# Kernel optimization log

Measured on AMD Instinct MI355X. Metric: run time of the kernel, lower is better.

Reference implementation:

```python
import jax, jax.numpy as jnp
import numpy as np

HID = 768
INTER = 3072
H = 12
DH = 64
N = 16384
W = 256   # attention_width
L = 512   # per-sequence length (power of 2, used via the uint32 bit-mask trick)


def rotate_every_two(x):
    x1 = x[..., ::2]
    x2 = x[..., 1::2]
    return jnp.stack((-x2, x1), axis=-1).reshape(x.shape)


def setup_inputs() -> dict:
    key = jax.random.key(0)
    ks = jax.random.split(key, 6)
    # GPT-J style interleaved rotary tables: sin/cos each value repeated twice
    inv_freq = 1.0 / (10000.0 ** (np.arange(0, DH, 2) / DH))  # [DH/2]
    ang = np.arange(N)[:, None] * inv_freq[None, :]           # [N, DH/2]
    pos_sin = jnp.asarray(np.repeat(np.sin(ang), 2, axis=-1), dtype=jnp.float32)
    pos_cos = jnp.asarray(np.repeat(np.cos(ang), 2, axis=-1), dtype=jnp.float32)
    return {
        "x": jax.random.normal(ks[0], (N, HID), dtype=jnp.float32),
        "normed_ages": jax.random.normal(ks[1], (N,), dtype=jnp.float32),
        "pos_sin": pos_sin,
        "pos_cos": pos_cos,
        "ln_scale": jnp.ones((HID,), dtype=jnp.float32),
        "ln_offset": jnp.zeros((HID,), dtype=jnp.float32),
        "w_in": jax.random.normal(ks[2], (HID, 3 * HID + INTER), dtype=jnp.float32) * 0.02,
        "b_in": jnp.zeros((3 * HID + INTER,), dtype=jnp.float32),
        "w_out": jax.random.normal(ks[3], (HID + INTER, HID), dtype=jnp.float32) * 0.02,
        "b_out": jnp.zeros((HID,), dtype=jnp.float32),
        "length": L,
    }


def reference(x, normed_ages, pos_sin, pos_cos, ln_scale, ln_offset,
              w_in, b_in, w_out, b_out, length):
    # LayerNorm (haiku: eps=1e-5, create_scale/offset)
    mu = jnp.mean(x, axis=-1, keepdims=True)
    var = jnp.var(x, axis=-1, keepdims=True)
    xn = (x - mu) * jax.lax.rsqrt(var + 1e-5) * ln_scale + ln_offset

    # fused QKV + FF projection (note: original computes x_with_ages but never uses it)
    mid = xn @ w_in + b_in
    q, k, v, ff = jnp.split(mid, [HID, 2 * HID, 3 * HID], axis=-1)

    def to_heads(t):  # [N, HID] -> [H, N, DH]
        return t.reshape(N, H, DH).transpose(1, 0, 2)

    q, k, v = to_heads(q), to_heads(k), to_heads(v)

    # rotary ('per_head'): sincos broadcast over heads
    sin, cos = pos_sin[None], pos_cos[None]
    q = q * cos + rotate_every_two(q) * sin
    k = k * cos + rotate_every_two(k) * sin

    # local (sliding-window, causal, within-sequence) attention, chunked by W
    C = W
    nc = N // C
    qc = q.reshape(H, nc, C, DH)
    kc = k.reshape(H, nc, C, DH)
    vc = v.reshape(H, nc, C, DH)
    kprev = jnp.concatenate([jnp.zeros_like(kc[:, :1]), kc[:, :-1]], axis=1)
    vprev = jnp.concatenate([jnp.zeros_like(vc[:, :1]), vc[:, :-1]], axis=1)
    kcat = jnp.concatenate([kprev, kc], axis=2)  # [H, nc, 2C, DH]
    vcat = jnp.concatenate([vprev, vc], axis=2)

    qi = (jnp.arange(nc) * C)[:, None] + jnp.arange(C)        # [nc, C]
    kj = (jnp.arange(nc) * C)[:, None] - C + jnp.arange(2 * C)  # [nc, 2C]
    lm = ~(jnp.uint32(length) - jnp.uint32(1))  # same bit-trick as the module
    same_seq = ((qi[:, :, None].astype(jnp.uint32) & lm) ==
                (jnp.maximum(kj, 0)[:, None, :].astype(jnp.uint32) & lm))
    d = qi[:, :, None] - kj[:, None, :]
    mask = (kj[:, None, :] >= 0) & (d >= 0) & (d < W) & same_seq  # [nc, C, 2C]

    scale = 1.0 / jnp.sqrt(jnp.float32(DH))
    scores = jnp.einsum('hncd,hnkd->hnck', qc, kcat) * scale
    scores = jnp.where(mask[None], scores, jnp.float32(-1e30))
    probs = jax.nn.softmax(scores, axis=-1)
    attn = jnp.einsum('hnck,hnkd->hncd', probs, vcat)

    attn = attn.reshape(H, N, DH).transpose(1, 0, 2).reshape(N, HID)
    combined = jnp.concatenate([attn, jax.nn.gelu(ff)], axis=-1)
    return xn + combined @ w_out + b_out
```

## Files before the change

### kernel.cpp

```cpp
#include <hip/hip_runtime.h>

#define N_TOK 16384
#define HIDN  768
#define MIDN  5376
#define COMBN 3840
#define NH    12
#define DHD   64
#define CHUNK 256
#define WIN   256

typedef short s16x8 __attribute__((ext_vector_type(8)));
typedef short s16x4 __attribute__((ext_vector_type(4)));
typedef float f32x4 __attribute__((ext_vector_type(4)));

__device__ __forceinline__ float bf2f(unsigned short u){
  union { unsigned u; float f; } x; x.u = ((unsigned)u) << 16; return x.f;
}
__device__ __forceinline__ unsigned short f2bf(float f){
  union { float f; unsigned u; } x; x.f = f;
  unsigned r = x.u + 0x7fffu + ((x.u >> 16) & 1u);
  return (unsigned short)(r >> 16);
}
__device__ __forceinline__ float gelu_fast(float x){
  float u = -1.5957691216057308f * (x + 0.044715f * x * x * x);
  return x / (1.f + __expf(u));
}
__device__ __forceinline__ void glds16(const void* g, void* l){
  __builtin_amdgcn_global_load_lds(
      (const __attribute__((address_space(1))) unsigned*)g,
      (__attribute__((address_space(3))) unsigned*)l, 16, 0, 0);
}

__global__ __launch_bounds__(256) void transpose_f2b(
    const float* __restrict__ in, unsigned short* __restrict__ out,
    int R, int Cc)
{
  __shared__ short t[64 * 72];
  const int tid = threadIdx.x;
  const int r0 = blockIdx.y * 64, c0 = blockIdx.x * 64;
  #pragma unroll
  for (int rep = 0; rep < 4; rep++){
    int v = tid + 256 * rep;
    int r = v >> 4, s = v & 15;
    float4 d = *(const float4*)(in + (size_t)(r0 + r) * Cc + c0 + s * 4);
    s16x4 o = { (short)f2bf(d.x), (short)f2bf(d.y), (short)f2bf(d.z), (short)f2bf(d.w) };
    *(s16x4*)(t + r * 72 + s * 4) = o;
  }
  __syncthreads();
  #pragma unroll
  for (int rep = 0; rep < 2; rep++){
    int v = tid + 256 * rep;
    int c = v & 63, s2 = v >> 6;
    s16x8 d;
    #pragma unroll
    for (int j = 0; j < 8; j++) d[j] = t[(s2 * 8 + j) * 72 + c];
    *(s16x8*)(out + (size_t)(c0 + c) * R + r0 + s2 * 8) = d;
  }
}

__global__ __launch_bounds__(256) void ln_kernel(
    const float* __restrict__ x, const float* __restrict__ sc,
    const float* __restrict__ ofs, unsigned short* __restrict__ xn)
{
  const int lane = threadIdx.x & 63, wv = threadIdx.x >> 6;
  const int row = blockIdx.x * 4 + wv;
  const float4* xr = (const float4*)(x + (size_t)row * HIDN);
  float4 vals[3];
  float sum = 0.f, sq = 0.f;
  #pragma unroll
  for (int j = 0; j < 3; j++){
    vals[j] = xr[lane + 64 * j];
    sum += vals[j].x + vals[j].y + vals[j].z + vals[j].w;
    sq  += vals[j].x * vals[j].x + vals[j].y * vals[j].y
         + vals[j].z * vals[j].z + vals[j].w * vals[j].w;
  }
  #pragma unroll
  for (int o = 1; o < 64; o <<= 1){ sum += __shfl_xor(sum, o); sq += __shfl_xor(sq, o); }
  const float mu = sum * (1.f / HIDN);
  const float rs = rsqrtf(fmaxf(sq * (1.f / HIDN) - mu * mu, 0.f) + 1e-5f);
  s16x4* xo = (s16x4*)(xn + (size_t)row * HIDN);
  const float4* scp = (const float4*)sc;
  const float4* ofp = (const float4*)ofs;
  #pragma unroll
  for (int j = 0; j < 3; j++){
    int p = lane + 64 * j;
    float4 s = scp[p], o = ofp[p];
    s16x4 w;
    w[0] = (short)f2bf((vals[j].x - mu) * rs * s.x + o.x);
    w[1] = (short)f2bf((vals[j].y - mu) * rs * s.y + o.y);
    w[2] = (short)f2bf((vals[j].z - mu) * rs * s.z + o.z);
    w[3] = (short)f2bf((vals[j].w - mu) * rs * s.w + o.w);
    xo[p] = w;
  }
}

__device__ __forceinline__ int swz(int row, int quad){
  return row * 64 + ((quad ^ ((row >> 1) & 3)) << 4);
}

__global__ __launch_bounds__(256, 2) void gemm1_k(
    const unsigned short* __restrict__ A, const unsigned short* __restrict__ BT,
    const float* __restrict__ bias,
    unsigned short* __restrict__ qb, unsigned short* __restrict__ kb,
    unsigned short* __restrict__ vb, unsigned short* __restrict__ comb)
{
  constexpr int K = HIDN;
  __shared__ short As[256 * 32];
  __shared__ short Bs[128 * 32];
  const int tid = threadIdx.x, lane = tid & 63, wv = tid >> 6;
  const int quad = lane >> 4, l15 = lane & 15;
  const int n0 = blockIdx.x * 128, m0 = blockIdx.y * 256;

  f32x4 acc[4][8];
  #pragma unroll
  for (int i = 0; i < 4; i++)
    #pragma unroll
    for (int j = 0; j < 8; j++) acc[i][j] = (f32x4){0.f,0.f,0.f,0.f};

  const int srow = tid >> 2;
  const int sseg = (tid & 3) ^ ((tid >> 3) & 3);
  const unsigned short* Ap = A  + (size_t)(m0 + srow) * K + sseg * 8;
  const unsigned short* Bp = BT + (size_t)(n0 + srow) * K + sseg * 8;
  const size_t rstep = (size_t)64 * K;
  char* AsB = ((char*)As) + tid * 16;
  char* BsB = ((char*)Bs) + tid * 16;

  int offA[4], offB[8];
  #pragma unroll
  for (int rt = 0; rt < 4; rt++) offA[rt] = swz(wv * 64 + rt * 16 + l15, quad);
  #pragma unroll
  for (int ct = 0; ct < 8; ct++) offB[ct] = swz(ct * 16 + l15, quad);

  for (int kt = 0; kt < K; kt += 32){
    __syncthreads();
    glds16(Ap + kt,             AsB);
    glds16(Ap + kt + rstep,     AsB + 4096);
    glds16(Ap + kt + 2 * rstep, AsB + 8192);
    glds16(Ap + kt + 3 * rstep, AsB + 12288);
    glds16(Bp + kt,             BsB);
    glds16(Bp + kt + rstep,     BsB + 4096);
    __syncthreads();
    s16x8 a[4], b[8];
    #pragma unroll
    for (int rt = 0; rt < 4; rt++) a[rt] = *(const s16x8*)((const char*)As + offA[rt]);
    #pragma unroll
    for (int ct = 0; ct < 8; ct++) b[ct] = *(const s16x8*)((const char*)Bs + offB[ct]);
    #pragma unroll
    for (int rt = 0; rt < 4; rt++)
      #pragma unroll
      for (int ct = 0; ct < 8; ct++)
        acc[rt][ct] = __builtin_amdgcn_mfma_f32_16x16x32_bf16(a[rt], b[ct], acc[rt][ct], 0, 0, 0);
  }

  unsigned short* dstb; int cb; bool isff = false;
  if (n0 < 768)       { dstb = qb;   cb = n0; }
  else if (n0 < 1536) { dstb = kb;   cb = n0 - 768; }
  else if (n0 < 2304) { dstb = vb;   cb = n0 - 1536; }
  else                { dstb = comb; cb = n0 - 1536; isff = true; }
  const int rowstride = isff ? COMBN : HIDN;

  #pragma unroll
  for (int ct = 0; ct < 8; ct++){
    const float bsv = bias[n0 + ct * 16 + l15];
    const int col = cb + ct * 16 + l15;
    #pragma unroll
    for (int rt = 0; rt < 4; rt++){
      #pragma unroll
      for (int r = 0; r < 4; r++){
        const int row = m0 + wv * 64 + rt * 16 + quad * 4 + r;
        float val = acc[rt][ct][r] + bsv;
        if (isff) val = gelu_fast(val);
        dstb[(size_t)row * rowstride + col] = f2bf(val);
      }
    }
  }
}

__global__ __launch_bounds__(256) void gemm2_k(
    const unsigned short* __restrict__ A, const unsigned short* __restrict__ BT,
    const float* __restrict__ bias, const unsigned short* __restrict__ xn,
    float* __restrict__ outp)
{
  constexpr int K = COMBN;
  __shared__ short As[128 * 32];
  __shared__ short Bs[128 * 32];
  const int tid = threadIdx.x, lane = tid & 63, wv = tid >> 6;
  const int quad = lane >> 4, l15 = lane & 15;
  const int m0 = blockIdx.y * 128, n0 = blockIdx.x * 128;
  const int wr = (wv >> 1) * 64, wc = (wv & 1) * 64;

  f32x4 acc[4][4];
  #pragma unroll
  for (int i = 0; i < 4; i++)
    #pragma unroll
    for (int j = 0; j < 4; j++) acc[i][j] = (f32x4){0.f,0.f,0.f,0.f};

  const int srow = tid >> 2;
  const int sseg = (tid & 3) ^ ((tid >> 3) & 3);
  const unsigned short* Ap = A  + (size_t)(m0 + srow) * K + sseg * 8;
  const unsigned short* Bp = BT + (size_t)(n0 + srow) * K + sseg * 8;
  const size_t rstep = (size_t)64 * K;
  char* AsB = ((char*)As) + tid * 16;
  char* BsB = ((char*)Bs) + tid * 16;

  int offA[4], offB[4];
  #pragma unroll
  for (int rt = 0; rt < 4; rt++) offA[rt] = swz(wr + rt * 16 + l15, quad);
  #pragma unroll
  for (int ct = 0; ct < 4; ct++) offB[ct] = swz(wc + ct * 16 + l15, quad);

  for (int kt = 0; kt < K; kt += 32){
    __syncthreads();
    glds16(Ap + kt,         AsB);
    glds16(Ap + kt + rstep, AsB + 4096);
    glds16(Bp + kt,         BsB);
    glds16(Bp + kt + rstep, BsB + 4096);
    __syncthreads();
    s16x8 a[4], b[4];
    #pragma unroll
    for (int rt = 0; rt < 4; rt++) a[rt] = *(const s16x8*)((const char*)As + offA[rt]);
    #pragma unroll
    for (int ct = 0; ct < 4; ct++) b[ct] = *(const s16x8*)((const char*)Bs + offB[ct]);
    #pragma unroll
    for (int rt = 0; rt < 4; rt++)
      #pragma unroll
      for (int ct = 0; ct < 4; ct++)
        acc[rt][ct] = __builtin_amdgcn_mfma_f32_16x16x32_bf16(a[rt], b[ct], acc[rt][ct], 0, 0, 0);
  }

  #pragma unroll
  for (int ct = 0; ct < 4; ct++){
    const int col = n0 + wc + ct * 16 + l15;
    const float bsv = bias[col];
    #pragma unroll
    for (int rt = 0; rt < 4; rt++){
      #pragma unroll
      for (int r = 0; r < 4; r++){
        const int row = m0 + wr + rt * 16 + quad * 4 + r;
        const size_t o = (size_t)row * HIDN + col;
        outp[o] = bf2f(xn[o]) + acc[rt][ct][r] + bsv;
      }
    }
  }
}

__global__ __launch_bounds__(384) void rope_qk(
    unsigned short* __restrict__ qb, unsigned short* __restrict__ kb,
    const float* __restrict__ psin, const float* __restrict__ pcos)
{
  __shared__ float ss[2048], cs[2048];
  const int tid = threadIdx.x, g = blockIdx.x;
  #pragma unroll
  for (int rep = 0; rep < 6; rep++){
    int idx = rep * 384 + tid;
    if (idx < 2048){
      int tok = idx >> 5, p = idx & 31;
      size_t gt = ((size_t)(g * 64 + tok)) * DHD + 2 * p;
      ss[idx] = psin[gt];
      cs[idx] = pcos[gt];
    }
  }
  __syncthreads();
  const int p = tid & 31;
  unsigned* q32 = (unsigned*)qb;
  unsigned* k32 = (unsigned*)kb;
  for (int tok = 0; tok < 64; tok++){
    const size_t a = ((size_t)(g * 64 + tok)) * 384 + tid;
    const float s = ss[tok * 32 + p], c0 = cs[tok * 32 + p];
    unsigned u = q32[a];
    float e = bf2f((unsigned short)(u & 0xffff));
    float d = bf2f((unsigned short)(u >> 16));
    q32[a] = (unsigned)f2bf((e * c0 - d * s) * 0.125f)
           | (((unsigned)f2bf((d * c0 + e * s) * 0.125f)) << 16);
    u = k32[a];
    e = bf2f((unsigned short)(u & 0xffff));
    d = bf2f((unsigned short)(u >> 16));
    k32[a] = (unsigned)f2bf(e * c0 - d * s)
           | (((unsigned)f2bf(d * c0 + e * s)) << 16);
  }
}

__global__ __launch_bounds__(256) void attn_kernel(
    const unsigned short* __restrict__ qb, const unsigned short* __restrict__ kb,
    const unsigned short* __restrict__ vb, unsigned short* __restrict__ comb,
    const int* __restrict__ lenp)
{
  __shared__ short Ks[2][64 * 72];
  __shared__ short Vt[2][64 * 64];
  __shared__ short Ps[4][16 * 72];
  const int tid = threadIdx.x, lane = tid & 63, wv = tid >> 6;
  const int quad = lane >> 4, l15 = lane & 15;
  const int h = blockIdx.y, c = blockIdx.x;
  const unsigned lm = ~((unsigned)lenp[0] - 1u);
  const int i0 = c * CHUNK + wv * 64;
  const unsigned short* qh = qb + h * DHD;
  const unsigned short* kh = kb + h * DHD;
  const unsigned short* vh = vb + h * DHD;

  s16x8 qf[4][2];
  #pragma unroll
  for (int rt = 0; rt < 4; rt++){
    const unsigned short* qr = qh + (size_t)(i0 + rt * 16 + l15) * HIDN;
    qf[rt][0] = *(const s16x8*)(qr + quad * 8);
    qf[rt][1] = *(const s16x8*)(qr + 32 + quad * 8);
  }

  f32x4 O[4][4];
  float mm[4][4], ll[4][4];
  #pragma unroll
  for (int rt = 0; rt < 4; rt++)
    #pragma unroll
    for (int j = 0; j < 4; j++){ O[rt][j] = (f32x4){0,0,0,0}; mm[rt][j] = -1e30f; ll[rt][j] = 0.f; }
  short* myP = &Ps[wv][0];

  const int skey = tid & 63, sseg = tid >> 6;
  const int jb0 = c * CHUNK - 256;
  s16x8 kr[2], vr[2];

  auto issue = [&](int jb){
    if (jb >= 0){
      const unsigned short* kp = kh + (size_t)(jb + skey) * HIDN + sseg * 16;
      const unsigned short* vp = vh + (size_t)(jb + skey) * HIDN + sseg * 16;
      kr[0] = *(const s16x8*)(kp);     kr[1] = *(const s16x8*)(kp + 8);
      vr[0] = *(const s16x8*)(vp);     vr[1] = *(const s16x8*)(vp + 8);
    } else {
      kr[0] = kr[1] = vr[0] = vr[1] = (s16x8){0,0,0,0,0,0,0,0};
    }
  };

  issue(jb0);
  for (int tb = 0; tb < 8; tb++){
    const int jb = jb0 + tb * 64;
    const int buf = tb & 1;
    short* Kb = &Ks[buf][0];
    short* Vb = &Vt[buf][0];
    *(s16x8*)(Kb + skey * 72 + sseg * 16)     = kr[0];
    *(s16x8*)(Kb + skey * 72 + sseg * 16 + 8) = kr[1];
    #pragma unroll
    for (int half = 0; half < 2; half++)
      #pragma unroll
      for (int j = 0; j < 8; j++){
        const int d = sseg * 16 + half * 8 + j;
        Vb[d * 64 + (((skey & 56) ^ ((d & 7) << 3)) | (skey & 7))] = vr[half][j];
      }
    if (tb < 7) issue(jb + 64);
    __syncthreads();

    const bool act = (jb >= 0) && (jb <= i0 + 63) && (jb + 63 >= i0 - 255) &&
                     (((unsigned)i0 & lm) == ((unsigned)jb & lm));
    if (!act) continue;

    #pragma unroll
    for (int rt = 0; rt < 4; rt++){
      const int ilo = i0 + rt * 16;
      if (ilo + 15 < jb || ilo - (jb + 63) >= WIN) continue;
      f32x4 sc[4];
      #pragma unroll
      for (int ct = 0; ct < 4; ct++){
        const short* kbase = Kb + (ct * 16 + l15) * 72 + quad * 8;
        const s16x8 b0 = *(const s16x8*)(kbase);
        const s16x8 b1 = *(const s16x8*)(kbase + 32);
        f32x4 a = (f32x4){0,0,0,0};
        a = __builtin_amdgcn_mfma_f32_16x16x32_bf16(qf[rt][0], b0, a, 0, 0, 0);
        a = __builtin_amdgcn_mfma_f32_16x16x32_bf16(qf[rt][1], b1, a, 0, 0, 0);
        sc[ct] = a;
      }
      float alph[4];
      #pragma unroll
      for (int r = 0; r < 4; r++){
        const int i = ilo + quad * 4 + r;
        #pragma unroll
        for (int ct = 0; ct < 4; ct++){
          const unsigned dd = (unsigned)(i - (jb + ct * 16 + l15));
          if (dd >= 256u) sc[ct][r] = -1e30f;
        }
        float mx = fmaxf(fmaxf(sc[0][r], sc[1][r]), fmaxf(sc[2][r], sc[3][r]));
        mx = fmaxf(mx, __shfl_xor(mx, 1));
        mx = fmaxf(mx, __shfl_xor(mx, 2));
        mx = fmaxf(mx, __shfl_xor(mx, 4));
        mx = fmaxf(mx, __shfl_xor(mx, 8));
        const float mnew = fmaxf(mm[rt][r], mx);
        alph[r] = __expf(mm[rt][r] - mnew);
        mm[rt][r] = mnew;
        float p0 = __expf(sc[0][r] - mnew);
        float p1 = __expf(sc[1][r] - mnew);
        float p2 = __expf(sc[2][r] - mnew);
        float p3 = __expf(sc[3][r] - mnew);
        sc[0][r] = p0; sc[1][r] = p1; sc[2][r] = p2; sc[3][r] = p3;
        float rsum = (p0 + p1) + (p2 + p3);
        rsum += __shfl_xor(rsum, 1);
        rsum += __shfl_xor(rsum, 2);
        rsum += __shfl_xor(rsum, 4);
        rsum += __shfl_xor(rsum, 8);
        ll[rt][r] = ll[rt][r] * alph[r] + rsum;
      }
      #pragma unroll
      for (int co = 0; co < 4; co++)
        #pragma unroll
        for (int r = 0; r < 4; r++) O[rt][co][r] *= alph[r];
      #pragma unroll
      for (int r = 0; r < 4; r++){
        const int prow = quad * 4 + r;
        #pragma unroll
        for (int ct = 0; ct < 4; ct++)
          myP[prow * 72 + ct * 16 + l15] = (short)f2bf(sc[ct][r]);
      }
      #pragma unroll
      for (int ks2 = 0; ks2 < 2; ks2++){
        const s16x8 pf = *(const s16x8*)(myP + l15 * 72 + ks2 * 32 + quad * 8);
        #pragma unroll
        for (int co = 0; co < 4; co++){
          const int d = co * 16 + l15;
          const s16x8 vf = *(const s16x8*)(Vb + d * 64 +
                              ((ks2 * 32 + quad * 8) ^ ((d & 7) << 3)));
          O[rt][co] = __builtin_amdgcn_mfma_f32_16x16x32_bf16(pf, vf, O[rt][co], 0, 0, 0);
        }
      }
    }
  }

  #pragma unroll
  for (int rt = 0; rt < 4; rt++)
    #pragma unroll
    for (int co = 0; co < 4; co++)
      #pragma unroll
      for (int r = 0; r < 4; r++){
        const int tok = i0 + rt * 16 + quad * 4 + r;
        comb[(size_t)tok * COMBN + h * DHD + co * 16 + l15] = f2bf(O[rt][co][r] / ll[rt][r]);
      }
}

extern "C" void kernel_launch(void* const* d_in, const int* in_sizes, int n_in,
                              void* d_out, int out_size, void* d_ws, size_t ws_size,
                              hipStream_t stream)
{
  const float* x     = (const float*)d_in[0];
  const float* psin  = (const float*)d_in[2];
  const float* pcos  = (const float*)d_in[3];
  const float* lns   = (const float*)d_in[4];
  const float* lno   = (const float*)d_in[5];
  const float* w_in  = (const float*)d_in[6];
  const float* b_in  = (const float*)d_in[7];
  const float* w_out = (const float*)d_in[8];
  const float* b_out = (const float*)d_in[9];
  const int*   lenp  = (const int*)d_in[10];
  float* out = (float*)d_out;

  char* ws = (char*)d_ws;
  size_t off = 0;
  unsigned short* xn    = (unsigned short*)(ws + off); off += (size_t)N_TOK * HIDN * 2;
  unsigned short* wInT  = (unsigned short*)(ws + off); off += (size_t)MIDN * HIDN * 2;
  unsigned short* wOutT = (unsigned short*)(ws + off); off += (size_t)HIDN * COMBN * 2;
  unsigned short* qbuf  = (unsigned short*)(ws + off); off += (size_t)N_TOK * HIDN * 2;
  unsigned short* kbuf  = (unsigned short*)(ws + off); off += (size_t)N_TOK * HIDN * 2;
  unsigned short* vbuf  = (unsigned short*)(ws + off); off += (size_t)N_TOK * HIDN * 2;
  unsigned short* comb  = (unsigned short*)(ws + off); off += (size_t)N_TOK * COMBN * 2;

  transpose_f2b<<<dim3(MIDN/64, HIDN/64), 256, 0, stream>>>(w_in, wInT, HIDN, MIDN);
  transpose_f2b<<<dim3(HIDN/64, COMBN/64), 256, 0, stream>>>(w_out, wOutT, COMBN, HIDN);
  ln_kernel<<<dim3(N_TOK/4), 256, 0, stream>>>(x, lns, lno, xn);
  gemm1_k<<<dim3(MIDN/128, N_TOK/256), 256, 0, stream>>>(
      xn, wInT, b_in, qbuf, kbuf, vbuf, comb);
  rope_qk<<<dim3(N_TOK/64), 384, 0, stream>>>(qbuf, kbuf, psin, pcos);
  attn_kernel<<<dim3(N_TOK/CHUNK, NH), 256, 0, stream>>>(
      qbuf, kbuf, vbuf, comb, lenp);
  gemm2_k<<<dim3(HIDN/128, N_TOK/128), 256, 0, stream>>>(
      comb, wOutT, b_out, xn, out);
}
```

Baseline: 699.1 us.

## Double-buffer LDS tiles in both GEMMs to overlap global loads with MFMA

Both GEMM kernels now hold two shared-memory tile buffers and issue the next K-tile's global-to-LDS loads before computing on the current tile. Explicit s_waitcnt vmcnt and s_barrier replace the two __syncthreads per iteration, so memory latency can overlap with MFMA work. This doubles LDS use per block, which may lower occupancy, especially in gemm1, which launches with two blocks per CU and already uses 24KB.

Measured after the change: 662.9 us. -5.2%, faster.

```diff
diff --git a/kernel.cpp b/kernel.cpp
--- a/kernel.cpp
+++ b/kernel.cpp
@@ -105,8 +105,9 @@
     unsigned short* __restrict__ vb, unsigned short* __restrict__ comb)
 {
   constexpr int K = HIDN;
-  __shared__ short As[256 * 32];
-  __shared__ short Bs[128 * 32];
+  constexpr int NKT = K / 32;
+  __shared__ short As[2][256 * 32];
+  __shared__ short Bs[2][128 * 32];
   const int tid = threadIdx.x, lane = tid & 63, wv = tid >> 6;
   const int quad = lane >> 4, l15 = lane & 15;
   const int n0 = blockIdx.x * 128, m0 = blockIdx.y * 256;
@@ -122,8 +123,8 @@
   const unsigned short* Ap = A  + (size_t)(m0 + srow) * K + sseg * 8;
   const unsigned short* Bp = BT + (size_t)(n0 + srow) * K + sseg * 8;
   const size_t rstep = (size_t)64 * K;
-  char* AsB = ((char*)As) + tid * 16;
-  char* BsB = ((char*)Bs) + tid * 16;
+  char* AsB[2] = { ((char*)As[0]) + tid * 16, ((char*)As[1]) + tid * 16 };
+  char* BsB[2] = { ((char*)Bs[0]) + tid * 16, ((char*)Bs[1]) + tid * 16 };
 
   int offA[4], offB[8];
   #pragma unroll
@@ -131,25 +132,46 @@
   #pragma unroll
   for (int ct = 0; ct < 8; ct++) offB[ct] = swz(ct * 16 + l15, quad);
 
-  for (int kt = 0; kt < K; kt += 32){
-    __syncthreads();
-    glds16(Ap + kt,             AsB);
-    glds16(Ap + kt + rstep,     AsB + 4096);
-    glds16(Ap + kt + 2 * rstep, AsB + 8192);
-    glds16(Ap + kt + 3 * rstep, AsB + 12288);
-    glds16(Bp + kt,             BsB);
-    glds16(Bp + kt + rstep,     BsB + 4096);
-    __syncthreads();
+  glds16(Ap,             AsB[0]);
+  glds16(Ap + rstep,     AsB[0] + 4096);
+  glds16(Ap + 2 * rstep, AsB[0] + 8192);
+  glds16(Ap + 3 * rstep, AsB[0] + 12288);
+  glds16(Bp,             BsB[0]);
+  glds16(Bp + rstep,     BsB[0] + 4096);
+
+  for (int t = 0; t < NKT; ++t){
+    const int buf = t & 1;
+    if (t + 1 < NKT){
+      const int kn = (t + 1) * 32;
+      char* Ad = AsB[buf ^ 1];
+      char* Bd = BsB[buf ^ 1];
+      glds16(Ap + kn,             Ad);
+      glds16(Ap + kn + rstep,     Ad + 4096);
+      glds16(Ap + kn + 2 * rstep, Ad + 8192);
+      glds16(Ap + kn + 3 * rstep, Ad + 12288);
+      glds16(Bp + kn,             Bd);
+      glds16(Bp + kn + rstep,     Bd + 4096);
+      asm volatile("s_waitcnt vmcnt(6)" ::: "memory");
+    } else {
+      asm volatile("s_waitcnt vmcnt(0)" ::: "memory");
+    }
+    asm volatile("s_barrier" ::: "memory");
+
+    const char* Ab = (const char*)As[buf];
+    const char* Bb = (const char*)Bs[buf];
     s16x8 a[4], b[8];
     #pragma unroll
-    for (int rt = 0; rt < 4; rt++) a[rt] = *(const s16x8*)((const char*)As + offA[rt]);
-    #pragma unroll
-    for (int ct = 0; ct < 8; ct++) b[ct] = *(const s16x8*)((const char*)Bs + offB[ct]);
+    for (int rt = 0; rt < 4; rt++) a[rt] = *(const s16x8*)(Ab + offA[rt]);
+    #pragma unroll
+    for (int ct = 0; ct < 8; ct++) b[ct] = *(const s16x8*)(Bb + offB[ct]);
     #pragma unroll
     for (int rt = 0; rt < 4; rt++)
       #pragma unroll
       for (int ct = 0; ct < 8; ct++)
         acc[rt][ct] = __builtin_amdgcn_mfma_f32_16x16x32_bf16(a[rt], b[ct], acc[rt][ct], 0, 0, 0);
+
+    asm volatile("s_waitcnt lgkmcnt(0)" ::: "memory");
+    asm volatile("s_barrier" ::: "memory");
   }
 
   unsigned short* dstb; int cb; bool isff = false;
@@ -182,8 +204,9 @@
     float* __restrict__ outp)
 {
   constexpr int K = COMBN;
-  __shared__ short As[128 * 32];
-  __shared__ short Bs[128 * 32];
+  constexpr int NKT = K / 32;
+  __shared__ short As[2][128 * 32];
+  __shared__ short Bs[2][128 * 32];
   const int tid = threadIdx.x, lane = tid & 63, wv = tid >> 6;
   const int quad = lane >> 4, l15 = lane & 15;
   const int m0 = blockIdx.y * 128, n0 = blockIdx.x * 128;
@@ -200,8 +223,8 @@
   const unsigned short* Ap = A  + (size_t)(m0 + srow) * K + sseg * 8;
   const unsigned short* Bp = BT + (size_t)(n0 + srow) * K + sseg * 8;
   const size_t rstep = (size_t)64 * K;
-  char* AsB = ((char*)As) + tid * 16;
-  char* BsB = ((char*)Bs) + tid * 16;
+  char* AsB[2] = { ((char*)As[0]) + tid * 16, ((char*)As[1]) + tid * 16 };
+  char* BsB[2] = { ((char*)Bs[0]) + tid * 16, ((char*)Bs[1]) + tid * 16 };
 
   int offA[4], offB[4];
   #pragma unroll
@@ -209,23 +232,42 @@
   #pragma unroll
   for (int ct = 0; ct < 4; ct++) offB[ct] = swz(wc + ct * 16 + l15, quad);
 
-  for (int kt = 0; kt < K; kt += 32){
-    __syncthreads();
-    glds16(Ap + kt,         AsB);
-    glds16(Ap + kt + rstep, AsB + 4096);
-    glds16(Bp + kt,         BsB);
-    glds16(Bp + kt + rstep, BsB + 4096);
-    __syncthreads();
+  glds16(Ap,         AsB[0]);
+  glds16(Ap + rstep, AsB[0] + 4096);
+  glds16(Bp,         BsB[0]);
+  glds16(Bp + rstep, BsB[0] + 4096);
+
+  for (int t = 0; t < NKT; ++t){
+    const int buf = t & 1;
+    if (t + 1 < NKT){
+      const int kn = (t + 1) * 32;
+      char* Ad = AsB[buf ^ 1];
+      char* Bd = BsB[buf ^ 1];
+      glds16(Ap + kn,         Ad);
+      glds16(Ap + kn + rstep, Ad + 4096);
+      glds16(Bp + kn,         Bd);
+      glds16(Bp + kn + rstep, Bd + 4096);
+      asm volatile("s_waitcnt vmcnt(4)" ::: "memory");
+    } else {
+      asm volatile("s_waitcnt vmcnt(0)" ::: "memory");
+    }
+    asm volatile("s_barrier" ::: "memory");
+
+    const char* Ab = (const char*)As[buf];
+    const char* Bb = (const char*)Bs[buf];
     s16x8 a[4], b[4];
     #pragma unroll
-    for (int rt = 0; rt < 4; rt++) a[rt] = *(const s16x8*)((const char*)As + offA[rt]);
-    #pragma unroll
-    for (int ct = 0; ct < 4; ct++) b[ct] = *(const s16x8*)((const char*)Bs + offB[ct]);
+    for (int rt = 0; rt < 4; rt++) a[rt] = *(const s16x8*)(Ab + offA[rt]);
+    #pragma unroll
+    for (int ct = 0; ct < 4; ct++) b[ct] = *(const s16x8*)(Bb + offB[ct]);
     #pragma unroll
     for (int rt = 0; rt < 4; rt++)
       #pragma unroll
       for (int ct = 0; ct < 4; ct++)
         acc[rt][ct] = __builtin_amdgcn_mfma_f32_16x16x32_bf16(a[rt], b[ct], acc[rt][ct], 0, 0, 0);
+
+    asm volatile("s_waitcnt lgkmcnt(0)" ::: "memory");
+    asm volatile("s_barrier" ::: "memory");
   }
 
   #pragma unroll
```

## Restructure both GEMMs into 256x256 double-buffered 8-wave tiles with prioritized MFMA phases

Applied to the files above, without the earlier changes.

Both projection GEMMs move to 256x256 output tiles with 512 threads (8 waves, 2x4 arrangement) and a 64-wide K step. Shared memory is double-buffered, and the next tile is prefetched with direct global-to-LDS loads overlapped with compute through vmcnt waits. The inner loop is split into four sub-phases with register reuse and s_setprio around the MFMA bursts. The aim is to hide global load latency and raise the compute-to-memory ratio. In exchange it uses 128KB of LDS per block, more accumulator registers, and launches fewer blocks: gemm1 gets 21 column blocks (MIDN/256), gemm2 only 3x64 blocks.

New measurement: 713.9 us. 2.1% more time.

```diff
diff --git a/kernel.cpp b/kernel.cpp
--- a/kernel.cpp
+++ b/kernel.cpp
@@ -94,62 +94,143 @@
   }
 }
 
-__device__ __forceinline__ int swz(int row, int quad){
-  return row * 64 + ((quad ^ ((row >> 1) & 3)) << 4);
-}
-
-__global__ __launch_bounds__(256, 2) void gemm1_k(
+
+__global__ __launch_bounds__(512, 2) void gemm1_k(
     const unsigned short* __restrict__ A, const unsigned short* __restrict__ BT,
     const float* __restrict__ bias,
     unsigned short* __restrict__ qb, unsigned short* __restrict__ kb,
     unsigned short* __restrict__ vb, unsigned short* __restrict__ comb)
 {
   constexpr int K = HIDN;
-  __shared__ short As[256 * 32];
-  __shared__ short Bs[128 * 32];
+  constexpr int T = K / 64;
+  __shared__ short As[2 * 256 * 64];
+  __shared__ short Bs[2 * 256 * 64];
   const int tid = threadIdx.x, lane = tid & 63, wv = tid >> 6;
   const int quad = lane >> 4, l15 = lane & 15;
-  const int n0 = blockIdx.x * 128, m0 = blockIdx.y * 256;
-
-  f32x4 acc[4][8];
-  #pragma unroll
-  for (int i = 0; i < 4; i++)
-    #pragma unroll
-    for (int j = 0; j < 8; j++) acc[i][j] = (f32x4){0.f,0.f,0.f,0.f};
-
-  const int srow = tid >> 2;
-  const int sseg = (tid & 3) ^ ((tid >> 3) & 3);
-  const unsigned short* Ap = A  + (size_t)(m0 + srow) * K + sseg * 8;
-  const unsigned short* Bp = BT + (size_t)(n0 + srow) * K + sseg * 8;
-  const size_t rstep = (size_t)64 * K;
-  char* AsB = ((char*)As) + tid * 16;
-  char* BsB = ((char*)Bs) + tid * 16;
-
-  int offA[4], offB[8];
-  #pragma unroll
-  for (int rt = 0; rt < 4; rt++) offA[rt] = swz(wv * 64 + rt * 16 + l15, quad);
-  #pragma unroll
-  for (int ct = 0; ct < 8; ct++) offB[ct] = swz(ct * 16 + l15, quad);
-
-  for (int kt = 0; kt < K; kt += 32){
-    __syncthreads();
-    glds16(Ap + kt,             AsB);
-    glds16(Ap + kt + rstep,     AsB + 4096);
-    glds16(Ap + kt + 2 * rstep, AsB + 8192);
-    glds16(Ap + kt + 3 * rstep, AsB + 12288);
-    glds16(Bp + kt,             BsB);
-    glds16(Bp + kt + rstep,     BsB + 4096);
-    __syncthreads();
-    s16x8 a[4], b[8];
-    #pragma unroll
-    for (int rt = 0; rt < 4; rt++) a[rt] = *(const s16x8*)((const char*)As + offA[rt]);
-    #pragma unroll
-    for (int ct = 0; ct < 8; ct++) b[ct] = *(const s16x8*)((const char*)Bs + offB[ct]);
-    #pragma unroll
-    for (int rt = 0; rt < 4; rt++)
-      #pragma unroll
-      for (int ct = 0; ct < 8; ct++)
-        acc[rt][ct] = __builtin_amdgcn_mfma_f32_16x16x32_bf16(a[rt], b[ct], acc[rt][ct], 0, 0, 0);
+  const int wr = wv >> 2, wc = wv & 3;
+  const int n0 = blockIdx.x * 256, m0 = blockIdx.y * 256;
+
+  f32x4 acc[8][4];
+  #pragma unroll
+  for (int i = 0; i < 8; i++)
+    #pragma unroll
+    for (int j = 0; j < 4; j++) acc[i][j] = (f32x4){0.f,0.f,0.f,0.f};
+
+  const int srow = tid >> 3;
+  const int koff = ((tid & 7) ^ ((tid >> 3) & 7)) * 8;
+  const unsigned short* Ap = A  + (size_t)(m0 + srow) * K + koff;
+  const unsigned short* Bp = BT + (size_t)(n0 + srow) * K + koff;
+  const size_t pstep = (size_t)64 * K;
+  char* const AsR = (char*)As;
+  char* const BsR = (char*)Bs;
+
+  const int seg0 = ((quad ^ (l15 & 7)) << 4);
+  const int seg1 = (((quad + 4) ^ (l15 & 7)) << 4);
+
+  auto stage = [&](int tt){
+    const int par = tt & 1;
+    char* Ad = AsR + par * 32768 + tid * 16;
+    char* Bd = BsR + par * 32768 + tid * 16;
+    const unsigned short* Asrc = Ap + tt * 64;
+    const unsigned short* Bsrc = Bp + tt * 64;
+    #pragma unroll
+    for (int part = 0; part < 4; part++)
+      glds16(Asrc + part * pstep, Ad + part * 8192);
+    #pragma unroll
+    for (int part = 0; part < 4; part++)
+      glds16(Bsrc + part * pstep, Bd + part * 8192);
+  };
+
+  stage(0);
+
+  s16x8 a[4][2], b[2][2];
+
+  #pragma unroll 2
+  for (int t = 0; t < T; t++){
+    const int par = t & 1;
+    const char* Ab = AsR + par * 32768;
+    const char* Bb = BsR + par * 32768;
+    if (t + 1 < T){
+      stage(t + 1);
+      asm volatile("s_waitcnt vmcnt(8)" ::: "memory");
+    } else {
+      asm volatile("s_waitcnt vmcnt(0)" ::: "memory");
+    }
+    asm volatile("s_barrier" ::: "memory");
+
+    #pragma unroll
+    for (int i = 0; i < 4; i++){
+      const char* rb = Ab + ((wr * 128 + i * 16 + l15) << 7);
+      a[i][0] = *(const s16x8*)(rb + seg0);
+      a[i][1] = *(const s16x8*)(rb + seg1);
+    }
+    #pragma unroll
+    for (int j = 0; j < 2; j++){
+      const char* rb = Bb + ((wc * 64 + j * 16 + l15) << 7);
+      b[j][0] = *(const s16x8*)(rb + seg0);
+      b[j][1] = *(const s16x8*)(rb + seg1);
+    }
+    __builtin_amdgcn_s_setprio(1);
+    #pragma unroll
+    for (int i = 0; i < 4; i++)
+      #pragma unroll
+      for (int j = 0; j < 2; j++){
+        acc[i][j] = __builtin_amdgcn_mfma_f32_16x16x32_bf16(a[i][0], b[j][0], acc[i][j], 0, 0, 0);
+        acc[i][j] = __builtin_amdgcn_mfma_f32_16x16x32_bf16(a[i][1], b[j][1], acc[i][j], 0, 0, 0);
+      }
+    __builtin_amdgcn_s_setprio(0);
+    asm volatile("s_barrier" ::: "memory");
+
+    #pragma unroll
+    for (int j = 0; j < 2; j++){
+      const char* rb = Bb + ((wc * 64 + (2 + j) * 16 + l15) << 7);
+      b[j][0] = *(const s16x8*)(rb + seg0);
+      b[j][1] = *(const s16x8*)(rb + seg1);
+    }
+    __builtin_amdgcn_s_setprio(1);
+    #pragma unroll
+    for (int i = 0; i < 4; i++)
+      #pragma unroll
+      for (int j = 0; j < 2; j++){
+        acc[i][2 + j] = __builtin_amdgcn_mfma_f32_16x16x32_bf16(a[i][0], b[j][0], acc[i][2 + j], 0, 0, 0);
+        acc[i][2 + j] = __builtin_amdgcn_mfma_f32_16x16x32_bf16(a[i][1], b[j][1], acc[i][2 + j], 0, 0, 0);
+      }
+    __builtin_amdgcn_s_setprio(0);
+    asm volatile("s_barrier" ::: "memory");
+
+    #pragma unroll
+    for (int i = 0; i < 4; i++){
+      const char* rb = Ab + ((wr * 128 + (4 + i) * 16 + l15) << 7);
+      a[i][0] = *(const s16x8*)(rb + seg0);
+      a[i][1] = *(const s16x8*)(rb + seg1);
+    }
+    __builtin_amdgcn_s_setprio(1);
+    #pragma unroll
+    for (int i = 0; i < 4; i++)
+      #pragma unroll
+      for (int j = 0; j < 2; j++){
+        acc[4 + i][2 + j] = __builtin_amdgcn_mfma_f32_16x16x32_bf16(a[i][0], b[j][0], acc[4 + i][2 + j], 0, 0, 0);
+        acc[4 + i][2 + j] = __builtin_amdgcn_mfma_f32_16x16x32_bf16(a[i][1], b[j][1], acc[4 + i][2 + j], 0, 0, 0);
+      }
+    __builtin_amdgcn_s_setprio(0);
+    asm volatile("s_barrier" ::: "memory");
+
+    #pragma unroll
+    for (int j = 0; j < 2; j++){
+      const char* rb = Bb + ((wc * 64 + j * 16 + l15) << 7);
+      b[j][0] = *(const s16x8*)(rb + seg0);
+      b[j][1] = *(const s16x8*)(rb + seg1);
+    }
+    __builtin_amdgcn_s_setprio(1);
+    #pragma unroll
+    for (int i = 0; i < 4; i++)
+      #pragma unroll
+      for (int j = 0; j < 2; j++){
+        acc[4 + i][j] = __builtin_amdgcn_mfma_f32_16x16x32_bf16(a[i][0], b[j][0], acc[4 + i][j], 0, 0, 0);
+        acc[4 + i][j] = __builtin_amdgcn_mfma_f32_16x16x32_bf16(a[i][1], b[j][1], acc[4 + i][j], 0, 0, 0);
+      }
+    __builtin_amdgcn_s_setprio(0);
+    asm volatile("s_barrier" ::: "memory");
   }
 
   unsigned short* dstb; int cb; bool isff = false;
@@ -160,15 +241,16 @@
   const int rowstride = isff ? COMBN : HIDN;
 
   #pragma unroll
-  for (int ct = 0; ct < 8; ct++){
-    const float bsv = bias[n0 + ct * 16 + l15];
-    const int col = cb + ct * 16 + l15;
-    #pragma unroll
-    for (int rt = 0; rt < 4; rt++){
+  for (int nf = 0; nf < 4; nf++){
+    const int colg = n0 + wc * 64 + nf * 16 + l15;
+    const float bsv = bias[colg];
+    const int col = cb + wc * 64 + nf * 16 + l15;
+    #pragma unroll
+    for (int mf = 0; mf < 8; mf++){
       #pragma unroll
       for (int r = 0; r < 4; r++){
-        const int row = m0 + wv * 64 + rt * 16 + quad * 4 + r;
-        float val = acc[rt][ct][r] + bsv;
+        const int row = m0 + wr * 128 + mf * 16 + quad * 4 + r;
+        float val = acc[mf][nf][r] + bsv;
         if (isff) val = gelu_fast(val);
         dstb[(size_t)row * rowstride + col] = f2bf(val);
       }
@@ -176,69 +258,154 @@
   }
 }
 
-__global__ __launch_bounds__(256) void gemm2_k(
+__global__ __launch_bounds__(512, 2) void gemm2_k(
     const unsigned short* __restrict__ A, const unsigned short* __restrict__ BT,
     const float* __restrict__ bias, const unsigned short* __restrict__ xn,
     float* __restrict__ outp)
 {
   constexpr int K = COMBN;
-  __shared__ short As[128 * 32];
-  __shared__ short Bs[128 * 32];
+  constexpr int T = K / 64;
+  __shared__ short As[2 * 256 * 64];
+  __shared__ short Bs[2 * 256 * 64];
   const int tid = threadIdx.x, lane = tid & 63, wv = tid >> 6;
   const int quad = lane >> 4, l15 = lane & 15;
-  const int m0 = blockIdx.y * 128, n0 = blockIdx.x * 128;
-  const int wr = (wv >> 1) * 64, wc = (wv & 1) * 64;
-
-  f32x4 acc[4][4];
-  #pragma unroll
-  for (int i = 0; i < 4; i++)
+  const int wr = wv >> 2, wc = wv & 3;
+  const int n0 = blockIdx.x * 256, m0 = blockIdx.y * 256;
+
+  f32x4 acc[8][4];
+  #pragma unroll
+  for (int i = 0; i < 8; i++)
     #pragma unroll
     for (int j = 0; j < 4; j++) acc[i][j] = (f32x4){0.f,0.f,0.f,0.f};
 
-  const int srow = tid >> 2;
-  const int sseg = (tid & 3) ^ ((tid >> 3) & 3);
-  const unsigned short* Ap = A  + (size_t)(m0 + srow) * K + sseg * 8;
-  const unsigned short* Bp = BT + (size_t)(n0 + srow) * K + sseg * 8;
-  const size_t rstep = (size_t)64 * K;
-  char* AsB = ((char*)As) + tid * 16;
-  char* BsB = ((char*)Bs) + tid * 16;
-
-  int offA[4], offB[4];
-  #pragma unroll
-  for (int rt = 0; rt < 4; rt++) offA[rt] = swz(wr + rt * 16 + l15, quad);
-  #pragma unroll
-  for (int ct = 0; ct < 4; ct++) offB[ct] = swz(wc + ct * 16 + l15, quad);
-
-  for (int kt = 0; kt < K; kt += 32){
-    __syncthreads();
-    glds16(Ap + kt,         AsB);
-    glds16(Ap + kt + rstep, AsB + 4096);
-    glds16(Bp + kt,         BsB);
-    glds16(Bp + kt + rstep, BsB + 4096);
-    __syncthreads();
-    s16x8 a[4], b[4];
-    #pragma unroll
-    for (int rt = 0; rt < 4; rt++) a[rt] = *(const s16x8*)((const char*)As + offA[rt]);
-    #pragma unroll
-    for (int ct = 0; ct < 4; ct++) b[ct] = *(const s16x8*)((const char*)Bs + offB[ct]);
-    #pragma unroll
-    for (int rt = 0; rt < 4; rt++)
-      #pragma unroll
-      for (int ct = 0; ct < 4; ct++)
-        acc[rt][ct] = __builtin_amdgcn_mfma_f32_16x16x32_bf16(a[rt], b[ct], acc[rt][ct], 0, 0, 0);
-  }
-
-  #pragma unroll
-  for (int ct = 0; ct < 4; ct++){
-    const int col = n0 + wc + ct * 16 + l15;
+  const int srow = tid >> 3;
+  const int koff = ((tid & 7) ^ ((tid >> 3) & 7)) * 8;
+  const unsigned short* Ap = A  + (size_t)(m0 + srow) * K + koff;
+  const unsigned short* Bp = BT + (size_t)(n0 + srow) * K + koff;
+  const size_t pstep = (size_t)64 * K;
+  char* const AsR = (char*)As;
+  char* const BsR = (char*)Bs;
+
+  const int seg0 = ((quad ^ (l15 & 7)) << 4);
+  const int seg1 = (((quad + 4) ^ (l15 & 7)) << 4);
+
+  auto stage = [&](int tt){
+    const int par = tt & 1;
+    char* Ad = AsR + par * 32768 + tid * 16;
+    char* Bd = BsR + par * 32768 + tid * 16;
+    const unsigned short* Asrc = Ap + tt * 64;
+    const unsigned short* Bsrc = Bp + tt * 64;
+    #pragma unroll
+    for (int part = 0; part < 4; part++)
+      glds16(Asrc + part * pstep, Ad + part * 8192);
+    #pragma unroll
+    for (int part = 0; part < 4; part++)
+      glds16(Bsrc + part * pstep, Bd + part * 8192);
+  };
+
+  stage(0);
+
+  s16x8 a[4][2], b[2][2];
+
+  #pragma unroll 2
+  for (int t = 0; t < T; t++){
+    const int par = t & 1;
+    const char* Ab = AsR + par * 32768;
+    const char* Bb = BsR + par * 32768;
+    if (t + 1 < T){
+      stage(t + 1);
+      asm volatile("s_waitcnt vmcnt(8)" ::: "memory");
+    } else {
+      asm volatile("s_waitcnt vmcnt(0)" ::: "memory");
+    }
+    asm volatile("s_barrier" ::: "memory");
+
+    #pragma unroll
+    for (int i = 0; i < 4; i++){
+      const char* rb = Ab + ((wr * 128 + i * 16 + l15) << 7);
+      a[i][0] = *(const s16x8*)(rb + seg0);
+      a[i][1] = *(const s16x8*)(rb + seg1);
+    }
+    #pragma unroll
+    for (int j = 0; j < 2; j++){
+      const char* rb = Bb + ((wc * 64 + j * 16 + l15) << 7);
+      b[j][0] = *(const s16x8*)(rb + seg0);
+      b[j][1] = *(const s16x8*)(rb + seg1);
+    }
+    __builtin_amdgcn_s_setprio(1);
+    #pragma unroll
+    for (int i = 0; i < 4; i++)
+      #pragma unroll
+      for (int j = 0; j < 2; j++){
+        acc[i][j] = __builtin_amdgcn_mfma_f32_16x16x32_bf16(a[i][0], b[j][0], acc[i][j], 0, 0, 0);
+        acc[i][j] = __builtin_amdgcn_mfma_f32_16x16x32_bf16(a[i][1], b[j][1], acc[i][j], 0, 0, 0);
+      }
+    __builtin_amdgcn_s_setprio(0);
+    asm volatile("s_barrier" ::: "memory");
+
+    #pragma unroll
+    for (int j = 0; j < 2; j++){
+      const char* rb = Bb + ((wc * 64 + (2 + j) * 16 + l15) << 7);
+      b[j][0] = *(const s16x8*)(rb + seg0);
+      b[j][1] = *(const s16x8*)(rb + seg1);
+    }
+    __builtin_amdgcn_s_setprio(1);
+    #pragma unroll
+    for (int i = 0; i < 4; i++)
+      #pragma unroll
+      for (int j = 0; j < 2; j++){
+        acc[i][2 + j] = __builtin_amdgcn_mfma_f32_16x16x32_bf16(a[i][0], b[j][0], acc[i][2 + j], 0, 0, 0);
+        acc[i][2 + j] = __builtin_amdgcn_mfma_f32_16x16x32_bf16(a[i][1], b[j][1], acc[i][2 + j], 0, 0, 0);
+      }
+    __builtin_amdgcn_s_setprio(0);
+    asm volatile("s_barrier" ::: "memory");
+
+    #pragma unroll
+    for (int i = 0; i < 4; i++){
+      const char* rb = Ab + ((wr * 128 + (4 + i) * 16 + l15) << 7);
+      a[i][0] = *(const s16x8*)(rb + seg0);
+      a[i][1] = *(const s16x8*)(rb + seg1);
+    }
+    __builtin_amdgcn_s_setprio(1);
+    #pragma unroll
+    for (int i = 0; i < 4; i++)
+      #pragma unroll
+      for (int j = 0; j < 2; j++){
+        acc[4 + i][2 + j] = __builtin_amdgcn_mfma_f32_16x16x32_bf16(a[i][0], b[j][0], acc[4 + i][2 + j], 0, 0, 0);
+        acc[4 + i][2 + j] = __builtin_amdgcn_mfma_f32_16x16x32_bf16(a[i][1], b[j][1], acc[4 + i][2 + j], 0, 0, 0);
+      }
+    __builtin_amdgcn_s_setprio(0);
+    asm volatile("s_barrier" ::: "memory");
+
+    #pragma unroll
+    for (int j = 0; j < 2; j++){
+      const char* rb = Bb + ((wc * 64 + j * 16 + l15) << 7);
+      b[j][0] = *(const s16x8*)(rb + seg0);
+      b[j][1] = *(const s16x8*)(rb + seg1);
+    }
+    __builtin_amdgcn_s_setprio(1);
+    #pragma unroll
+    for (int i = 0; i < 4; i++)
+      #pragma unroll
+      for (int j = 0; j < 2; j++){
+        acc[4 + i][j] = __builtin_amdgcn_mfma_f32_16x16x32_bf16(a[i][0], b[j][0], acc[4 + i][j], 0, 0, 0);
+        acc[4 + i][j] = __builtin_amdgcn_mfma_f32_16x16x32_bf16(a[i][1], b[j][1], acc[4 + i][j], 0, 0, 0);
+      }
+    __builtin_amdgcn_s_setprio(0);
+    asm volatile("s_barrier" ::: "memory");
+  }
+
+  #pragma unroll
+  for (int nf = 0; nf < 4; nf++){
+    const int col = n0 + wc * 64 + nf * 16 + l15;
     const float bsv = bias[col];
     #pragma unroll
-    for (int rt = 0; rt < 4; rt++){
+    for (int mf = 0; mf < 8; mf++){
       #pragma unroll
       for (int r = 0; r < 4; r++){
-        const int row = m0 + wr + rt * 16 + quad * 4 + r;
+        const int row = m0 + wr * 128 + mf * 16 + quad * 4 + r;
         const size_t o = (size_t)row * HIDN + col;
-        outp[o] = bf2f(xn[o]) + acc[rt][ct][r] + bsv;
+        outp[o] = bf2f(xn[o]) + acc[mf][nf][r] + bsv;
       }
     }
   }
@@ -459,11 +626,11 @@
   transpose_f2b<<<dim3(MIDN/64, HIDN/64), 256, 0, stream>>>(w_in, wInT, HIDN, MIDN);
   transpose_f2b<<<dim3(HIDN/64, COMBN/64), 256, 0, stream>>>(w_out, wOutT, COMBN, HIDN);
   ln_kernel<<<dim3(N_TOK/4), 256, 0, stream>>>(x, lns, lno, xn);
-  gemm1_k<<<dim3(MIDN/128, N_TOK/256), 256, 0, stream>>>(
+  gemm1_k<<<dim3(MIDN/256, N_TOK/256), 512, 0, stream>>>(
       xn, wInT, b_in, qbuf, kbuf, vbuf, comb);
   rope_qk<<<dim3(N_TOK/64), 384, 0, stream>>>(qbuf, kbuf, psin, pcos);
   attn_kernel<<<dim3(N_TOK/CHUNK, NH), 256, 0, stream>>>(
       qbuf, kbuf, vbuf, comb, lenp);
-  gemm2_k<<<dim3(HIDN/128, N_TOK/128), 256, 0, stream>>>(
+  gemm2_k<<<dim3(HIDN/256, N_TOK/256), 512, 0, stream>>>(
       comb, wOutT, b_out, xn, out);
 }
```

## Replace both GEMMs with a shared 4-stage LDS-pipelined 256x256 tile routine

Applied to the files above, without the earlier changes.

Both projection GEMMs now use a common templated main loop. It keeps a four-deep ring of shared-memory buffers filled by direct global-to-LDS loads issued two K-steps ahead. Hand-placed waitcnt/barrier instructions and MFMA priority bumps overlap memory traffic with matrix math and drop the two full barriers per K-step. Tiles grow to 256x256 with 512 threads and 8x4 MFMA fragments per wave, which raises reuse. The cost is heavy LDS use (128 KB per block) and far fewer blocks for the output GEMM (192 blocks on a 256-CU device), so part of the device may sit idle.

Measured after the change: 715.2 us. +2.3%, slower.

```diff
diff --git a/kernel.cpp b/kernel.cpp
--- a/kernel.cpp
+++ b/kernel.cpp
@@ -94,63 +94,106 @@
   }
 }
 
-__device__ __forceinline__ int swz(int row, int quad){
-  return row * 64 + ((quad ^ ((row >> 1) & 3)) << 4);
-}
-
-__global__ __launch_bounds__(256, 2) void gemm1_k(
+template<int K>
+__device__ __forceinline__ void gemm_pipe(
+    const unsigned short* __restrict__ A, const unsigned short* __restrict__ BT,
+    short* AsBuf, short* BsBuf,
+    int tid, int quad, int l15, int wr, int wc, int m0, int n0,
+    f32x4 acc[8][4])
+{
+  constexpr int T = K / 32;
+  constexpr int BUFSZ = 256 * 32;
+
+  const int srow = tid >> 2;
+  const int ksw  = ((tid & 3) ^ ((tid >> 3) & 3)) * 8;
+  const unsigned short* Ap = A  + (size_t)(m0 + srow) * K + ksw;
+  const unsigned short* Bp = BT + (size_t)(n0 + srow) * K + ksw;
+  const size_t halfstep = (size_t)128 * K;
+
+  auto stage = [&](int tt){
+    char* Ad = ((char*)(AsBuf + (size_t)(tt & 3) * BUFSZ)) + tid * 16;
+    char* Bd = ((char*)(BsBuf + (size_t)(tt & 3) * BUFSZ)) + tid * 16;
+    const unsigned short* Asrc = Ap + tt * 32;
+    const unsigned short* Bsrc = Bp + tt * 32;
+    glds16(Asrc,            Ad);
+    glds16(Asrc + halfstep, Ad + 8192);
+    glds16(Bsrc,            Bd);
+    glds16(Bsrc + halfstep, Bd + 8192);
+  };
+
+  const int seg = ((quad ^ ((l15 >> 1) & 3)) << 4);
+  int offA[8], offB[4];
+  #pragma unroll
+  for (int mf = 0; mf < 8; mf++) offA[mf] = (wr * 128 + mf * 16 + l15) * 64 + seg;
+  #pragma unroll
+  for (int nf = 0; nf < 4; nf++) offB[nf] = (wc * 64 + nf * 16 + l15) * 64 + seg;
+
+  stage(0); stage(1);
+  asm volatile("s_waitcnt vmcnt(4)" ::: "memory");
+  asm volatile("s_barrier" ::: "memory");
+
+  s16x8 a[4], a2[4], b[4];
+  {
+    const char* A0 = (const char*)AsBuf;
+    const char* B0 = (const char*)BsBuf;
+    #pragma unroll
+    for (int i = 0; i < 4; i++) a[i] = *(const s16x8*)(A0 + offA[i]);
+    #pragma unroll
+    for (int j = 0; j < 4; j++) b[j] = *(const s16x8*)(B0 + offB[j]);
+  }
+
+  #pragma unroll 4
+  for (int t = 0; t < T; t++){
+    if (t + 2 < T) stage(t + 2);
+    const char* Ab = (const char*)(AsBuf + (size_t)(t & 3) * BUFSZ);
+    #pragma unroll
+    for (int i = 0; i < 4; i++) a2[i] = *(const s16x8*)(Ab + offA[4 + i]);
+    __builtin_amdgcn_s_setprio(1);
+    #pragma unroll
+    for (int i = 0; i < 4; i++)
+      #pragma unroll
+      for (int j = 0; j < 4; j++)
+        acc[i][j] = __builtin_amdgcn_mfma_f32_16x16x32_bf16(a[i], b[j], acc[i][j], 0, 0, 0);
+    #pragma unroll
+    for (int i = 0; i < 4; i++)
+      #pragma unroll
+      for (int j = 0; j < 4; j++)
+        acc[4 + i][j] = __builtin_amdgcn_mfma_f32_16x16x32_bf16(a2[i], b[j], acc[4 + i][j], 0, 0, 0);
+    __builtin_amdgcn_s_setprio(0);
+    if (t + 1 < T){
+      if (t + 2 < T){ asm volatile("s_waitcnt vmcnt(4)" ::: "memory"); }
+      else          { asm volatile("s_waitcnt vmcnt(0)" ::: "memory"); }
+      asm volatile("s_barrier" ::: "memory");
+      const char* An = (const char*)(AsBuf + (size_t)((t + 1) & 3) * BUFSZ);
+      const char* Bn = (const char*)(BsBuf + (size_t)((t + 1) & 3) * BUFSZ);
+      #pragma unroll
+      for (int i = 0; i < 4; i++) a[i] = *(const s16x8*)(An + offA[i]);
+      #pragma unroll
+      for (int j = 0; j < 4; j++) b[j] = *(const s16x8*)(Bn + offB[j]);
+    }
+  }
+}
+
+__global__ __launch_bounds__(512, 2) void gemm1_k(
     const unsigned short* __restrict__ A, const unsigned short* __restrict__ BT,
     const float* __restrict__ bias,
     unsigned short* __restrict__ qb, unsigned short* __restrict__ kb,
     unsigned short* __restrict__ vb, unsigned short* __restrict__ comb)
 {
-  constexpr int K = HIDN;
-  __shared__ short As[256 * 32];
-  __shared__ short Bs[128 * 32];
+  __shared__ short As[4][256 * 32];
+  __shared__ short Bs[4][256 * 32];
   const int tid = threadIdx.x, lane = tid & 63, wv = tid >> 6;
   const int quad = lane >> 4, l15 = lane & 15;
-  const int n0 = blockIdx.x * 128, m0 = blockIdx.y * 256;
-
-  f32x4 acc[4][8];
-  #pragma unroll
-  for (int i = 0; i < 4; i++)
-    #pragma unroll
-    for (int j = 0; j < 8; j++) acc[i][j] = (f32x4){0.f,0.f,0.f,0.f};
-
-  const int srow = tid >> 2;
-  const int sseg = (tid & 3) ^ ((tid >> 3) & 3);
-  const unsigned short* Ap = A  + (size_t)(m0 + srow) * K + sseg * 8;
-  const unsigned short* Bp = BT + (size_t)(n0 + srow) * K + sseg * 8;
-  const size_t rstep = (size_t)64 * K;
-  char* AsB = ((char*)As) + tid * 16;
-  char* BsB = ((char*)Bs) + tid * 16;
-
-  int offA[4], offB[8];
-  #pragma unroll
-  for (int rt = 0; rt < 4; rt++) offA[rt] = swz(wv * 64 + rt * 16 + l15, quad);
-  #pragma unroll
-  for (int ct = 0; ct < 8; ct++) offB[ct] = swz(ct * 16 + l15, quad);
-
-  for (int kt = 0; kt < K; kt += 32){
-    __syncthreads();
-    glds16(Ap + kt,             AsB);
-    glds16(Ap + kt + rstep,     AsB + 4096);
-    glds16(Ap + kt + 2 * rstep, AsB + 8192);
-    glds16(Ap + kt + 3 * rstep, AsB + 12288);
-    glds16(Bp + kt,             BsB);
-    glds16(Bp + kt + rstep,     BsB + 4096);
-    __syncthreads();
-    s16x8 a[4], b[8];
-    #pragma unroll
-    for (int rt = 0; rt < 4; rt++) a[rt] = *(const s16x8*)((const char*)As + offA[rt]);
-    #pragma unroll
-    for (int ct = 0; ct < 8; ct++) b[ct] = *(const s16x8*)((const char*)Bs + offB[ct]);
-    #pragma unroll
-    for (int rt = 0; rt < 4; rt++)
-      #pragma unroll
-      for (int ct = 0; ct < 8; ct++)
-        acc[rt][ct] = __builtin_amdgcn_mfma_f32_16x16x32_bf16(a[rt], b[ct], acc[rt][ct], 0, 0, 0);
-  }
+  const int wr = wv >> 2, wc = wv & 3;
+  const int n0 = blockIdx.x * 256, m0 = blockIdx.y * 256;
+
+  f32x4 acc[8][4];
+  #pragma unroll
+  for (int i = 0; i < 8; i++)
+    #pragma unroll
+    for (int j = 0; j < 4; j++) acc[i][j] = (f32x4){0.f,0.f,0.f,0.f};
+
+  gemm_pipe<HIDN>(A, BT, &As[0][0], &Bs[0][0], tid, quad, l15, wr, wc, m0, n0, acc);
 
   unsigned short* dstb; int cb; bool isff = false;
   if (n0 < 768)       { dstb = qb;   cb = n0; }
@@ -158,17 +201,17 @@
   else if (n0 < 2304) { dstb = vb;   cb = n0 - 1536; }
   else                { dstb = comb; cb = n0 - 1536; isff = true; }
   const int rowstride = isff ? COMBN : HIDN;
-
-  #pragma unroll
-  for (int ct = 0; ct < 8; ct++){
-    const float bsv = bias[n0 + ct * 16 + l15];
-    const int col = cb + ct * 16 + l15;
-    #pragma unroll
-    for (int rt = 0; rt < 4; rt++){
+  #pragma unroll
+  for (int nf = 0; nf < 4; nf++){
+    const int colg = n0 + wc * 64 + nf * 16 + l15;
+    const float bsv = bias[colg];
+    const int col = cb + wc * 64 + nf * 16 + l15;
+    #pragma unroll
+    for (int mf = 0; mf < 8; mf++){
       #pragma unroll
       for (int r = 0; r < 4; r++){
-        const int row = m0 + wv * 64 + rt * 16 + quad * 4 + r;
-        float val = acc[rt][ct][r] + bsv;
+        const int row = m0 + wr * 128 + mf * 16 + quad * 4 + r;
+        float val = acc[mf][nf][r] + bsv;
         if (isff) val = gelu_fast(val);
         dstb[(size_t)row * rowstride + col] = f2bf(val);
       }
@@ -176,69 +219,37 @@
   }
 }
 
-__global__ __launch_bounds__(256) void gemm2_k(
+__global__ __launch_bounds__(512, 2) void gemm2_k(
     const unsigned short* __restrict__ A, const unsigned short* __restrict__ BT,
     const float* __restrict__ bias, const unsigned short* __restrict__ xn,
     float* __restrict__ outp)
 {
-  constexpr int K = COMBN;
-  __shared__ short As[128 * 32];
-  __shared__ short Bs[128 * 32];
+  __shared__ short As[4][256 * 32];
+  __shared__ short Bs[4][256 * 32];
   const int tid = threadIdx.x, lane = tid & 63, wv = tid >> 6;
   const int quad = lane >> 4, l15 = lane & 15;
-  const int m0 = blockIdx.y * 128, n0 = blockIdx.x * 128;
-  const int wr = (wv >> 1) * 64, wc = (wv & 1) * 64;
-
-  f32x4 acc[4][4];
-  #pragma unroll
-  for (int i = 0; i < 4; i++)
+  const int wr = wv >> 2, wc = wv & 3;
+  const int n0 = blockIdx.x * 256, m0 = blockIdx.y * 256;
+
+  f32x4 acc[8][4];
+  #pragma unroll
+  for (int i = 0; i < 8; i++)
     #pragma unroll
     for (int j = 0; j < 4; j++) acc[i][j] = (f32x4){0.f,0.f,0.f,0.f};
 
-  const int srow = tid >> 2;
-  const int sseg = (tid & 3) ^ ((tid >> 3) & 3);
-  const unsigned short* Ap = A  + (size_t)(m0 + srow) * K + sseg * 8;
-  const unsigned short* Bp = BT + (size_t)(n0 + srow) * K + sseg * 8;
-  const size_t rstep = (size_t)64 * K;
-  char* AsB = ((char*)As) + tid * 16;
-  char* BsB = ((char*)Bs) + tid * 16;
-
-  int offA[4], offB[4];
-  #pragma unroll
-  for (int rt = 0; rt < 4; rt++) offA[rt] = swz(wr + rt * 16 + l15, quad);
-  #pragma unroll
-  for (int ct = 0; ct < 4; ct++) offB[ct] = swz(wc + ct * 16 + l15, quad);
-
-  for (int kt = 0; kt < K; kt += 32){
-    __syncthreads();
-    glds16(Ap + kt,         AsB);
-    glds16(Ap + kt + rstep, AsB + 4096);
-    glds16(Bp + kt,         BsB);
-    glds16(Bp + kt + rstep, BsB + 4096);
-    __syncthreads();
-    s16x8 a[4], b[4];
-    #pragma unroll
-    for (int rt = 0; rt < 4; rt++) a[rt] = *(const s16x8*)((const char*)As + offA[rt]);
-    #pragma unroll
-    for (int ct = 0; ct < 4; ct++) b[ct] = *(const s16x8*)((const char*)Bs + offB[ct]);
-    #pragma unroll
-    for (int rt = 0; rt < 4; rt++)
-      #pragma unroll
-      for (int ct = 0; ct < 4; ct++)
-        acc[rt][ct] = __builtin_amdgcn_mfma_f32_16x16x32_bf16(a[rt], b[ct], acc[rt][ct], 0, 0, 0);
-  }
-
-  #pragma unroll
-  for (int ct = 0; ct < 4; ct++){
-    const int col = n0 + wc + ct * 16 + l15;
+  gemm_pipe<COMBN>(A, BT, &As[0][0], &Bs[0][0], tid, quad, l15, wr, wc, m0, n0, acc);
+
+  #pragma unroll
+  for (int nf = 0; nf < 4; nf++){
+    const int col = n0 + wc * 64 + nf * 16 + l15;
     const float bsv = bias[col];
     #pragma unroll
-    for (int rt = 0; rt < 4; rt++){
+    for (int mf = 0; mf < 8; mf++){
       #pragma unroll
       for (int r = 0; r < 4; r++){
-        const int row = m0 + wr + rt * 16 + quad * 4 + r;
+        const int row = m0 + wr * 128 + mf * 16 + quad * 4 + r;
         const size_t o = (size_t)row * HIDN + col;
-        outp[o] = bf2f(xn[o]) + acc[rt][ct][r] + bsv;
+        outp[o] = bf2f(xn[o]) + acc[mf][nf][r] + bsv;
       }
     }
   }
@@ -360,10 +371,10 @@
         const short* kbase = Kb + (ct * 16 + l15) * 72 + quad * 8;
         const s16x8 b0 = *(const s16x8*)(kbase);
         const s16x8 b1 = *(const s16x8*)(kbase + 32);
-        f32x4 a = (f32x4){0,0,0,0};
-        a = __builtin_amdgcn_mfma_f32_16x16x32_bf16(qf[rt][0], b0, a, 0, 0, 0);
-        a = __builtin_amdgcn_mfma_f32_16x16x32_bf16(qf[rt][1], b1, a, 0, 0, 0);
-        sc[ct] = a;
+        f32x4 aa = (f32x4){0,0,0,0};
+        aa = __builtin_amdgcn_mfma_f32_16x16x32_bf16(qf[rt][0], b0, aa, 0, 0, 0);
+        aa = __builtin_amdgcn_mfma_f32_16x16x32_bf16(qf[rt][1], b1, aa, 0, 0, 0);
+        sc[ct] = aa;
       }
       float alph[4];
       #pragma unroll
@@ -459,11 +470,11 @@
   transpose_f2b<<<dim3(MIDN/64, HIDN/64), 256, 0, stream>>>(w_in, wInT, HIDN, MIDN);
   transpose_f2b<<<dim3(HIDN/64, COMBN/64), 256, 0, stream>>>(w_out, wOutT, COMBN, HIDN);
   ln_kernel<<<dim3(N_TOK/4), 256, 0, stream>>>(x, lns, lno, xn);
-  gemm1_k<<<dim3(MIDN/128, N_TOK/256), 256, 0, stream>>>(
+  gemm1_k<<<dim3(MIDN/256, N_TOK/256), 512, 0, stream>>>(
       xn, wInT, b_in, qbuf, kbuf, vbuf, comb);
   rope_qk<<<dim3(N_TOK/64), 384, 0, stream>>>(qbuf, kbuf, psin, pcos);
   attn_kernel<<<dim3(N_TOK/CHUNK, NH), 256, 0, stream>>>(
       qbuf, kbuf, vbuf, comb, lenp);
-  gemm2_k<<<dim3(HIDN/128, N_TOK/128), 256, 0, stream>>>(
+  gemm2_k<<<dim3(HIDN/256, N_TOK/256), 512, 0, stream>>>(
       comb, wOutT, b_out, xn, out);
 }
```
